# Optimization experiments

Measured on AMD Instinct MI355X. Metric: run time of the kernel, lower is better.

## Reference

```python
import jax, jax.numpy as jnp
import numpy as np

DIM = 32
NUM_BLOCKS = 6
XP_DIM = 16
TP_DIM = 8


def _init_lin(key, fan_in, fan_out):
    kw, kb = jax.random.split(key)
    s = 1.0 / np.sqrt(fan_in)
    W = jax.random.uniform(kw, (fan_in, fan_out), jnp.float32, -s, s)
    b = jax.random.uniform(kb, (fan_out,), jnp.float32, -s, s)
    return W, b


def setup_inputs() -> dict:
    key = jax.random.key(0)
    ks = jax.random.split(key, 24)
    B, N = 16, 256
    inp = {
        'coords': jax.random.normal(ks[0], (B, N, 2), jnp.float32),
        'x_params': jax.random.normal(ks[1], (B, 8, 2), jnp.float32),
        't_params': jax.random.normal(ks[2], (B, TP_DIM), jnp.float32),
    }
    # xp2ex: DNN([16,32,32],'sin')
    inp['xp2ex_W1'], inp['xp2ex_b1'] = _init_lin(ks[3], XP_DIM, DIM)
    inp['xp2ex_W2'], inp['xp2ex_b2'] = _init_lin(ks[4], DIM, DIM)
    # tp2et: DNN([8,32,32],'sin')
    inp['tp2et_W1'], inp['tp2et_b1'] = _init_lin(ks[5], TP_DIM, DIM)
    inp['tp2et_W2'], inp['tp2et_b2'] = _init_lin(ks[6], DIM, DIM)
    # initial hidden states (learnable; random instead of zeros for testing)
    inp['h0'] = 0.1 * jax.random.normal(ks[7], (1, DIM), jnp.float32)
    inp['gh0'] = 0.1 * jax.random.normal(ks[8], (1, DIM), jnp.float32)
    fWh, fbh, fWz, fbz = [], [], [], []
    for i in range(NUM_BLOCKS):
        W, b = _init_lin(ks[9 + i], DIM, DIM); fWh.append(W); fbh.append(b)
        W, b = _init_lin(jax.random.fold_in(ks[9 + i], 1), 2 + DIM, DIM); fWz.append(W); fbz.append(b)
    inp['f_Wh'], inp['f_bh'] = jnp.stack(fWh), jnp.stack(fbh)
    inp['f_Wz'], inp['f_bz'] = jnp.stack(fWz), jnp.stack(fbz)
    gWh, gbh, gWz, gbz = [], [], [], []
    for i in range(NUM_BLOCKS):
        W, b = _init_lin(ks[15 + i], DIM, DIM); gWh.append(W); gbh.append(b)
        W, b = _init_lin(jax.random.fold_in(ks[15 + i], 1), DIM + DIM, DIM); gWz.append(W); gbz.append(b)
    inp['g_Wh'], inp['g_bh'] = jnp.stack(gWh), jnp.stack(gbh)
    inp['g_Wz'], inp['g_bz'] = jnp.stack(gWz), jnp.stack(gbz)
    # d: SymmetricInitDNN([32,1],'identity') -> single linear
    inp['d_W'], inp['d_b'] = _init_lin(ks[21], DIM, 1)
    return inp


def reference(coords, x_params, t_params,
              xp2ex_W1, xp2ex_b1, xp2ex_W2, xp2ex_b2,
              tp2et_W1, tp2et_b1, tp2et_W2, tp2et_b2,
              h0, gh0,
              f_Wh, f_bh, f_Wz, f_bz,
              g_Wh, g_bh, g_Wz, g_bz,
              d_W, d_b):
    B, N = coords.shape[0], coords.shape[1]
    x = coords[..., 0:1]   # (B, N, 1)
    t = coords[..., 1:2]   # (B, N, 1)
    # conditioning embeddings (2-layer sin MLPs, linear output)
    xp = x_params.reshape(B, -1)                                   # (B, 16)
    ex = jnp.sin(xp @ xp2ex_W1 + xp2ex_b1) @ xp2ex_W2 + xp2ex_b2   # (B, 32)
    et = jnp.sin(t_params @ tp2et_W1 + tp2et_b1) @ tp2et_W2 + tp2et_b2  # (B, 32)
    # broadcast to (B, Nt, Nx, .) grid
    tr = jnp.broadcast_to(t[:, :, None, :], (B, N, N, 1))
    xr = jnp.broadcast_to(x[:, None, :, :], (B, N, N, 1))
    etu = jnp.broadcast_to(et[:, None, None, :], (B, N, N, DIM))
    ztpx = jnp.concatenate([xr, tr, etu], axis=-1)  # (B, N, N, 34)

    def block_step(h, w):
        Wh, bh, Wz, bz = w
        return jnp.sin(h @ Wh + bh + h_cond @ Wz + bz), None

    # f-stream: modulated-SIREN blocks conditioned on (x, t, et)
    h_cond = ztpx
    h = jnp.broadcast_to(h0[None, None], (B, N, N, DIM))
    h, _ = jax.lax.scan(block_step, h, (f_Wh, f_bh, f_Wz, f_bz))
    # g-stream: conditioned on (h, ex)
    ex_b = jnp.broadcast_to(ex[:, None, None, :], (B, N, N, DIM))
    h_cond = jnp.concatenate([h, ex_b], axis=-1)  # (B, N, N, 64)
    gh = jnp.broadcast_to(gh0[None, None], (B, N, N, DIM))
    gh, _ = jax.lax.scan(block_step, gh, (g_Wh, g_bh, g_Wz, g_bz))
    u_pred = gh @ d_W + d_b  # (B, N, N, 1)
    return u_pred
```

## Files before the change

kernel.cpp:

```cpp
#include <hip/hip_runtime.h>

#define DIM 32
#define NB  6
#define INV2PI 0.15915494309189535f

typedef __attribute__((ext_vector_type(8)))  _Float16 half8;
typedef __attribute__((ext_vector_type(16))) float floatx16;

union H8I4 { half8 h; int i[4]; };

__device__ __forceinline__ int pkrne(float a, float b) {
    _Float16 h0 = (_Float16)a, h1 = (_Float16)b;
    unsigned short u0, u1;
    __builtin_memcpy(&u0, &h0, 2); __builtin_memcpy(&u1, &h1, 2);
    return (int)(u0 | ((unsigned)u1 << 16));
}
#if __has_builtin(__builtin_amdgcn_cvt_pkrtz)
__device__ __forceinline__ int pkrtz(float a, float b) {
    auto h = __builtin_amdgcn_cvt_pkrtz(a, b);
    int r; __builtin_memcpy(&r, &h, 4); return r;
}
#else
#define pkrtz pkrne
#endif

__device__ __forceinline__ int Pmap(int s, int h, int j) { return 16*s + 8*(j>>2) + 4*h + (j&3); }
__device__ __forceinline__ int Qmap(int p)               { int r = p & 15, h = p >> 4; return 8*(r>>2) + 4*h + (r&3); }

#define MFMA(a, b, c) __builtin_amdgcn_mfma_f32_32x32x16_f16((a), (b), (c), 0, 0, 0)

__device__ __forceinline__ void sinsplit(const floatx16& acc, half8& b1, half8& b2) {
    H8I4 n1, n2;
    #pragma unroll
    for (int q = 0; q < 4; ++q) {
        n1.i[q] = pkrtz(__builtin_amdgcn_sinf(acc[2*q]),
                        __builtin_amdgcn_sinf(acc[2*q+1]));
        n2.i[q] = pkrtz(__builtin_amdgcn_sinf(acc[8+2*q]),
                        __builtin_amdgcn_sinf(acc[8+2*q+1]));
    }
    b1 = n1.h; b2 = n2.h;
}

#define LDS_BYTES 40064

__global__ __launch_bounds__(512, 4) void sep_mfma(
    const float* __restrict__ coords,
    const float* __restrict__ x_params,
    const float* __restrict__ t_params,
    const float* __restrict__ xW1, const float* __restrict__ xb1,
    const float* __restrict__ xW2, const float* __restrict__ xb2,
    const float* __restrict__ tW1, const float* __restrict__ tb1,
    const float* __restrict__ tW2, const float* __restrict__ tb2,
    const float* __restrict__ h0,  const float* __restrict__ gh0,
    const float* __restrict__ f_Wh, const float* __restrict__ f_bh,
    const float* __restrict__ f_Wz, const float* __restrict__ f_bz,
    const float* __restrict__ g_Wh, const float* __restrict__ g_bh,
    const float* __restrict__ g_Wz, const float* __restrict__ g_bz,
    const float* __restrict__ d_W,  const float* __restrict__ d_b,
    float* __restrict__ out)
{
    extern __shared__ char smem[];
    float* sdWp   = (float*)smem;
    float* shx    = sdWp + 32;
    float* sht    = shx + 32;
    float* sex    = sht + 32;
    float* set_   = sex + 32;
    unsigned short* sImg  = (unsigned short*)(set_ + 32);
    unsigned short* sInj  = sImg + 16384;
    unsigned short* sGnj  = sInj + 1536;
    unsigned short* sZero = sGnj + 1536;

    const int tid = threadIdx.x;
    const int b   = blockIdx.x >> 6;
    const int ig  = (blockIdx.x >> 1) & 31;
    const int jg  = blockIdx.x & 1;

    if (tid < 32) {
        float a = xb1[tid];
        for (int k = 0; k < 16; ++k) a = fmaf(x_params[b * 16 + k], xW1[k * 32 + tid], a);
        shx[tid] = __sinf(a);
    } else if (tid < 64) {
        int d = tid - 32;
        float a = tb1[d];
        for (int k = 0; k < 8; ++k) a = fmaf(t_params[b * 8 + k], tW1[k * 32 + d], a);
        sht[d] = __sinf(a);
    }
    if (tid < 128) ((int*)sZero)[tid] = 0;
    {
        int* sImgI = (int*)sImg;
        for (int ii = tid; ii < 8192; ii += 512) {
            int region = ii >> 9;
            int r = ii & 511;
            int s = r >> 8, t = r & 255;
            int lane = t >> 2, jj2 = t & 3;
            int m = lane & 31, hg = lane >> 5;
            int c0 = 16*s + 8*(jj2 >> 1) + 4*hg + 2*(jj2 & 1);
            float w0, w1;
            if (region < 5)       { int l = region + 1;  w0 = f_Wh[(l*32 + c0)*32 + m]; w1 = f_Wh[(l*32 + c0 + 1)*32 + m]; }
            else if (region < 10) { int l = region - 4;  w0 = g_Wh[(l*32 + c0)*32 + m]; w1 = g_Wh[(l*32 + c0 + 1)*32 + m]; }
            else                  { int l = region - 10; w0 = g_Wz[(l*64 + c0)*32 + m]; w1 = g_Wz[(l*64 + c0 + 1)*32 + m]; }
            sImgI[ii] = pkrne(w0 * INV2PI, w1 * INV2PI);
        }
    }
    __syncthreads();

    if (tid < 32) {
        float a0 = xb2[tid], a1 = 0.f, a2 = 0.f, a3 = 0.f;
        #pragma unroll
        for (int c = 0; c < 32; c += 4) {
            a0 = fmaf(shx[c],     xW2[(c)     * 32 + tid], a0);
            a1 = fmaf(shx[c + 1], xW2[(c + 1) * 32 + tid], a1);
            a2 = fmaf(shx[c + 2], xW2[(c + 2) * 32 + tid], a2);
            a3 = fmaf(shx[c + 3], xW2[(c + 3) * 32 + tid], a3);
        }
        sex[tid] = (a0 + a1) + (a2 + a3);
    } else if (tid < 64) {
        int d = tid - 32;
        float a0 = tb2[d], a1 = 0.f, a2 = 0.f, a3 = 0.f;
        #pragma unroll
        for (int c = 0; c < 32; c += 4) {
            a0 = fmaf(sht[c],     tW2[(c)     * 32 + d], a0);
            a1 = fmaf(sht[c + 1], tW2[(c + 1) * 32 + d], a1);
            a2 = fmaf(sht[c + 2], tW2[(c + 2) * 32 + d], a2);
            a3 = fmaf(sht[c + 3], tW2[(c + 3) * 32 + d], a3);
        }
        set_[d] = (a0 + a1) + (a2 + a3);
    }
    if (tid < 192) {
        int l = tid >> 5, m = tid & 31;
        float z0 = f_Wz[(l * 34 + 0) * 32 + m] * INV2PI;
        float z1 = f_Wz[(l * 34 + 1) * 32 + m] * INV2PI;
        _Float16 h0_ = (_Float16)z0; float z0h = (float)h0_, z0l = z0 - z0h;
        _Float16 h1_ = (_Float16)z1; float z1h = (float)h1_, z1l = z1 - z1h;
        int* p = (int*)sInj + 4 * tid;
        p[0] = pkrne(z0h, z0h);
        p[1] = pkrne(z0l, z1h);
        p[2] = pkrne(z1h, z1l);
        int* q = (int*)sGnj + 4 * tid;
        q[0] = 0; q[1] = 0; q[2] = 0;
    }
    if (tid < 32) sdWp[tid] = d_W[Qmap(tid)];
    __syncthreads();

    if (tid < 192) {
        int l = tid >> 5, m = tid & 31;
        float a0 = f_bh[l * 32 + m] + f_bz[l * 32 + m], a1 = 0.f, a2 = 0.f, a3 = 0.f;
        #pragma unroll
        for (int c = 0; c < 32; c += 4) {
            a0 = fmaf(set_[c],     f_Wz[(l * 34 + 2 + c) * 32 + m], a0);
            a1 = fmaf(set_[c + 1], f_Wz[(l * 34 + 3 + c) * 32 + m], a1);
            a2 = fmaf(set_[c + 2], f_Wz[(l * 34 + 4 + c) * 32 + m], a2);
            a3 = fmaf(set_[c + 3], f_Wz[(l * 34 + 5 + c) * 32 + m], a3);
        }
        float a = (a0 + a1) + (a2 + a3);
        if (l == 0) {
            float b0 = 0.f, b1 = 0.f, b2 = 0.f, b3 = 0.f;
            #pragma unroll
            for (int c = 0; c < 32; c += 4) {
                b0 = fmaf(h0[c],     f_Wh[(c)     * 32 + m], b0);
                b1 = fmaf(h0[c + 1], f_Wh[(c + 1) * 32 + m], b1);
                b2 = fmaf(h0[c + 2], f_Wh[(c + 2) * 32 + m], b2);
                b3 = fmaf(h0[c + 3], f_Wh[(c + 3) * 32 + m], b3);
            }
            a += (b0 + b1) + (b2 + b3);
        }
        a *= INV2PI;
        _Float16 aH_ = (_Float16)a; float aH = (float)aH_, aL = a - aH;
        ((int*)sInj)[4 * tid + 3] = pkrne(aH, aL);

        float g0 = g_bh[l * 32 + m] + g_bz[l * 32 + m], g1 = 0.f, g2 = 0.f, g3 = 0.f;
        #pragma unroll
        for (int c = 0; c < 32; c += 4) {
            g0 = fmaf(sex[c],     g_Wz[(l * 64 + 32 + c)     * 32 + m], g0);
            g1 = fmaf(sex[c + 1], g_Wz[(l * 64 + 32 + c + 1) * 32 + m], g1);
            g2 = fmaf(sex[c + 2], g_Wz[(l * 64 + 32 + c + 2) * 32 + m], g2);
            g3 = fmaf(sex[c + 3], g_Wz[(l * 64 + 32 + c + 3) * 32 + m], g3);
        }
        float g = (g0 + g1) + (g2 + g3);
        if (l == 0) {
            float c0_ = 0.f, c1_ = 0.f, c2_ = 0.f, c3_ = 0.f;
            #pragma unroll
            for (int c = 0; c < 32; c += 4) {
                c0_ = fmaf(gh0[c],     g_Wh[(c)     * 32 + m], c0_);
                c1_ = fmaf(gh0[c + 1], g_Wh[(c + 1) * 32 + m], c1_);
                c2_ = fmaf(gh0[c + 2], g_Wh[(c + 2) * 32 + m], c2_);
                c3_ = fmaf(gh0[c + 3], g_Wh[(c + 3) * 32 + m], c3_);
            }
            g += (c0_ + c1_) + (c2_ + c3_);
        }
        g *= INV2PI;
        _Float16 gH_ = (_Float16)g; float gH = (float)gH_, gL = g - gH;
        ((int*)sGnj)[4 * tid + 3] = pkrne(gH, gL);
    }
    __syncthreads();

    const int lane = tid & 63, wave = tid >> 6;
    const int i = ig * 8 + wave;
    const int e = lane & 31, hk = lane >> 5;
    const int pb = hk * 16;
    const float ti = coords[(b * 256 + i) * 2 + 1];
    const float db = d_b[0];

    float th_, tl_;
    { _Float16 h = (_Float16)ti; th_ = (float)h; tl_ = ti - th_; }

    const unsigned short* injbase = hk ? sZero : (sInj + e * 8);
    const unsigned short* gnjbase = hk ? sZero : (sGnj + e * 8);
    const int injstep = hk ? 0 : 256;

    floatx16 zc;
    #pragma unroll
    for (int r = 0; r < 16; ++r) zc[r] = 0.0f;

    #pragma unroll 1
    for (int t = 0; t < 4; ++t) {
        const int tile = jg * 4 + t;
        const int j = tile * 32 + e;
        const float xj = coords[(b * 256 + j) * 2];

        float xh_, xl_;
        { _Float16 h = (_Float16)xj; xh_ = (float)h; xl_ = xj - xh_; }
        H8I4 xtb;
        xtb.i[0] = pkrtz(xh_, xl_);
        xtb.i[1] = pkrtz(xh_, th_);
        xtb.i[2] = pkrtz(tl_, th_);
        xtb.i[3] = 0x3C003C00;
        const half8 xtB = xtb.h;

        floatx16 acc;
        half8 hB1, hB2;
        const unsigned short* ip = injbase;
        const unsigned short* gp = gnjbase;

        {
            half8 ia = *(const half8*)ip; ip += injstep;
            acc = MFMA(ia, xtB, zc);
            sinsplit(acc, hB1, hB2);
        }
        for (int l = 1; l < NB; ++l) {
            __builtin_amdgcn_sched_barrier(0);
            const unsigned short* base = &sImg[((l - 1) * 2) * 512 + lane * 8];
            half8 ia  = *(const half8*)ip; ip += injstep;
            half8 ah0 = *(const half8*)(base);
            half8 ah1 = *(const half8*)(base + 512);
            floatx16 z;
            z = MFMA(ia, xtB, zc);
            z = MFMA(ah0, hB1, z);
            acc = MFMA(ah1, hB2, z);
            sinsplit(acc, hB1, hB2);
        }

        half8 gB1, gB2;
        {
            __builtin_amdgcn_sched_barrier(0);
            const unsigned short* bz = &sImg[10240 + lane * 8];
            half8 gi  = *(const half8*)gp; gp += injstep;
            half8 wz0 = *(const half8*)(bz);
            half8 wz1 = *(const half8*)(bz + 512);
            floatx16 z;
            z = MFMA(gi, xtB, zc);
            z = MFMA(wz0, hB1, z);
            acc = MFMA(wz1, hB2, z);
            sinsplit(acc, gB1, gB2);
        }
        for (int l = 1; l < NB; ++l) {
            __builtin_amdgcn_sched_barrier(0);
            const unsigned short* bz = &sImg[10240 + (l * 2) * 512 + lane * 8];
            const unsigned short* bh = &sImg[5120 + ((l - 1) * 2) * 512 + lane * 8];
            half8 gi  = *(const half8*)gp; gp += injstep;
            half8 wz0 = *(const half8*)(bz);
            half8 wz1 = *(const half8*)(bz + 512);
            half8 wh0 = *(const half8*)(bh);
            half8 wh1 = *(const half8*)(bh + 512);
            floatx16 z;
            z = MFMA(gi, xtB, zc);
            z = MFMA(wz0, hB1, z);
            z = MFMA(wz1, hB2, z);
            z = MFMA(wh0, gB1, z);
            acc = MFMA(wh1, gB2, z);
            if (l < NB - 1) sinsplit(acc, gB1, gB2);
        }

        float u = 0.0f;
        #pragma unroll
        for (int r = 0; r < 16; ++r) u = fmaf(__builtin_amdgcn_sinf(acc[r]), sdWp[pb + r], u);
        u += __shfl_xor(u, 32);
        if (hk == 0) out[(b * 256 + i) * 256 + j] = u + db;
    }
}

extern "C" void kernel_launch(void* const* d_in, const int* in_sizes, int n_in,
                              void* d_out, int out_size, void* d_ws, size_t ws_size,
                              hipStream_t stream) {
    const float* coords   = (const float*)d_in[0];
    const float* x_params = (const float*)d_in[1];
    const float* t_params = (const float*)d_in[2];
    const float* xW1 = (const float*)d_in[3];
    const float* xb1 = (const float*)d_in[4];
    const float* xW2 = (const float*)d_in[5];
    const float* xb2 = (const float*)d_in[6];
    const float* tW1 = (const float*)d_in[7];
    const float* tb1 = (const float*)d_in[8];
    const float* tW2 = (const float*)d_in[9];
    const float* tb2 = (const float*)d_in[10];
    const float* h0  = (const float*)d_in[11];
    const float* gh0 = (const float*)d_in[12];
    const float* f_Wh = (const float*)d_in[13];
    const float* f_bh = (const float*)d_in[14];
    const float* f_Wz = (const float*)d_in[15];
    const float* f_bz = (const float*)d_in[16];
    const float* g_Wh = (const float*)d_in[17];
    const float* g_bh = (const float*)d_in[18];
    const float* g_Wz = (const float*)d_in[19];
    const float* g_bz = (const float*)d_in[20];
    const float* d_W  = (const float*)d_in[21];
    const float* d_b  = (const float*)d_in[22];

    hipFuncSetAttribute((const void*)sep_mfma,
                        hipFuncAttributeMaxDynamicSharedMemorySize, LDS_BYTES);

    sep_mfma<<<1024, 512, LDS_BYTES, stream>>>(
        coords, x_params, t_params, xW1, xb1, xW2, xb2, tW1, tb1, tW2, tb2,
        h0, gh0, f_Wh, f_bh, f_Wz, f_bz, g_Wh, g_bh, g_Wz, g_bz, d_W, d_b,
        (float*)d_out);
}
```

Measured before the change: 153.7 us.

## Interleave two independent column tiles per wave to hide MFMA and sin latency

Each block now covers all 256 columns of a row group, so the grid is halved and the per-block LDS weight setup is amortised over twice as much work. Inside the loop each wave processes two 32-column tiles, A and B, whose MFMA chains and sin activations are interleaved so the two dependency chains overlap. The injection MFMA is moved to the end of each chain. Launch bounds drop to 2 blocks per SM, which allows more registers for the doubled accumulators but lowers occupancy and gives fewer blocks for load balance.

After: 148.8 us. 3.2% less time.

```diff
diff --git a/kernel.cpp b/kernel.cpp
--- a/kernel.cpp
+++ b/kernel.cpp
@@ -43,7 +43,7 @@
 
 #define LDS_BYTES 40064
 
-__global__ __launch_bounds__(512, 4) void sep_mfma(
+__global__ __launch_bounds__(512, 2) void sep_mfma(
     const float* __restrict__ coords,
     const float* __restrict__ x_params,
     const float* __restrict__ t_params,
@@ -71,9 +71,8 @@
     unsigned short* sZero = sGnj + 1536;
 
     const int tid = threadIdx.x;
-    const int b   = blockIdx.x >> 6;
-    const int ig  = (blockIdx.x >> 1) & 31;
-    const int jg  = blockIdx.x & 1;
+    const int b   = blockIdx.x >> 5;
+    const int ig  = blockIdx.x & 31;
 
     if (tid < 32) {
         float a = xb1[tid];
@@ -208,84 +207,114 @@
     const unsigned short* gnjbase = hk ? sZero : (sGnj + e * 8);
     const int injstep = hk ? 0 : 256;
 
-    floatx16 zc;
-    #pragma unroll
-    for (int r = 0; r < 16; ++r) zc[r] = 0.0f;
-
     #pragma unroll 1
     for (int t = 0; t < 4; ++t) {
-        const int tile = jg * 4 + t;
-        const int j = tile * 32 + e;
-        const float xj = coords[(b * 256 + j) * 2];
-
-        float xh_, xl_;
-        { _Float16 h = (_Float16)xj; xh_ = (float)h; xl_ = xj - xh_; }
-        H8I4 xtb;
-        xtb.i[0] = pkrtz(xh_, xl_);
-        xtb.i[1] = pkrtz(xh_, th_);
-        xtb.i[2] = pkrtz(tl_, th_);
-        xtb.i[3] = 0x3C003C00;
-        const half8 xtB = xtb.h;
-
-        floatx16 acc;
-        half8 hB1, hB2;
+        const int jA = (2 * t) * 32 + e;
+        const int jB = jA + 32;
+        const float xjA = coords[(b * 256 + jA) * 2];
+        const float xjB = coords[(b * 256 + jB) * 2];
+
+        half8 btA, btB;
+        {
+            float xh_, xl_;
+            { _Float16 h = (_Float16)xjA; xh_ = (float)h; xl_ = xjA - xh_; }
+            H8I4 u;
+            u.i[0] = pkrtz(xh_, xl_);
+            u.i[1] = pkrtz(xh_, th_);
+            u.i[2] = pkrtz(tl_, th_);
+            u.i[3] = 0x3C003C00;
+            btA = u.h;
+            { _Float16 h = (_Float16)xjB; xh_ = (float)h; xl_ = xjB - xh_; }
+            u.i[0] = pkrtz(xh_, xl_);
+            u.i[1] = pkrtz(xh_, th_);
+            u.i[2] = pkrtz(tl_, th_);
+            u.i[3] = 0x3C003C00;
+            btB = u.h;
+        }
+
+        floatx16 accA, accB;
+        half8 hA1, hA2, hB1, hB2;
         const unsigned short* ip = injbase;
         const unsigned short* gp = gnjbase;
 
         {
             half8 ia = *(const half8*)ip; ip += injstep;
-            acc = MFMA(ia, xtB, zc);
-            sinsplit(acc, hB1, hB2);
+            floatx16 zA, zB;
+            #pragma unroll
+            for (int r = 0; r < 16; ++r) { zA[r] = 0.0f; zB[r] = 0.0f; }
+            accA = MFMA(ia, btA, zA);
+            accB = MFMA(ia, btB, zB);
+            sinsplit(accA, hA1, hA2);
+            sinsplit(accB, hB1, hB2);
         }
         for (int l = 1; l < NB; ++l) {
             __builtin_amdgcn_sched_barrier(0);
             const unsigned short* base = &sImg[((l - 1) * 2) * 512 + lane * 8];
-            half8 ia  = *(const half8*)ip; ip += injstep;
             half8 ah0 = *(const half8*)(base);
             half8 ah1 = *(const half8*)(base + 512);
-            floatx16 z;
-            z = MFMA(ia, xtB, zc);
-            z = MFMA(ah0, hB1, z);
-            acc = MFMA(ah1, hB2, z);
-            sinsplit(acc, hB1, hB2);
-        }
-
-        half8 gB1, gB2;
+            half8 ia  = *(const half8*)ip; ip += injstep;
+            floatx16 zA, zB;
+            #pragma unroll
+            for (int r = 0; r < 16; ++r) { zA[r] = 0.0f; zB[r] = 0.0f; }
+            zA = MFMA(ah0, hA1, zA);  zB = MFMA(ah0, hB1, zB);
+            zA = MFMA(ah1, hA2, zA);  zB = MFMA(ah1, hB2, zB);
+            accA = MFMA(ia, btA, zA); accB = MFMA(ia, btB, zB);
+            sinsplit(accA, hA1, hA2);
+            sinsplit(accB, hB1, hB2);
+        }
+
+        half8 gA1, gA2, gB1, gB2;
         {
             __builtin_amdgcn_sched_barrier(0);
             const unsigned short* bz = &sImg[10240 + lane * 8];
-            half8 gi  = *(const half8*)gp; gp += injstep;
             half8 wz0 = *(const half8*)(bz);
             half8 wz1 = *(const half8*)(bz + 512);
-            floatx16 z;
-            z = MFMA(gi, xtB, zc);
-            z = MFMA(wz0, hB1, z);
-            acc = MFMA(wz1, hB2, z);
-            sinsplit(acc, gB1, gB2);
+            half8 gi  = *(const half8*)gp; gp += injstep;
+            floatx16 zA, zB;
+            #pragma unroll
+            for (int r = 0; r < 16; ++r) { zA[r] = 0.0f; zB[r] = 0.0f; }
+            zA = MFMA(wz0, hA1, zA);  zB = MFMA(wz0, hB1, zB);
+            zA = MFMA(wz1, hA2, zA);  zB = MFMA(wz1, hB2, zB);
+            accA = MFMA(gi, btA, zA); accB = MFMA(gi, btB, zB);
+            sinsplit(accA, gA1, gA2);
+            sinsplit(accB, gB1, gB2);
         }
         for (int l = 1; l < NB; ++l) {
             __builtin_amdgcn_sched_barrier(0);
             const unsigned short* bz = &sImg[10240 + (l * 2) * 512 + lane * 8];
             const unsigned short* bh = &sImg[5120 + ((l - 1) * 2) * 512 + lane * 8];
-            half8 gi  = *(const half8*)gp; gp += injstep;
             half8 wz0 = *(const half8*)(bz);
             half8 wz1 = *(const half8*)(bz + 512);
             half8 wh0 = *(const half8*)(bh);
             half8 wh1 = *(const half8*)(bh + 512);
-            floatx16 z;
-            z = MFMA(gi, xtB, zc);
-            z = MFMA(wz0, hB1, z);
-            z = MFMA(wz1, hB2, z);
-            z = MFMA(wh0, gB1, z);
-            acc = MFMA(wh1, gB2, z);
-            if (l < NB - 1) sinsplit(acc, gB1, gB2);
-        }
-
-        float u = 0.0f;
-        #pragma unroll
-        for (int r = 0; r < 16; ++r) u = fmaf(__builtin_amdgcn_sinf(acc[r]), sdWp[pb + r], u);
-        u += __shfl_xor(u, 32);
-        if (hk == 0) out[(b * 256 + i) * 256 + j] = u + db;
+            half8 gi  = *(const half8*)gp; gp += injstep;
+            floatx16 zA, zB;
+            #pragma unroll
+            for (int r = 0; r < 16; ++r) { zA[r] = 0.0f; zB[r] = 0.0f; }
+            zA = MFMA(wz0, hA1, zA);  zB = MFMA(wz0, hB1, zB);
+            zA = MFMA(wz1, hA2, zA);  zB = MFMA(wz1, hB2, zB);
+            zA = MFMA(wh0, gA1, zA);  zB = MFMA(wh0, gB1, zB);
+            zA = MFMA(wh1, gA2, zA);  zB = MFMA(wh1, gB2, zB);
+            accA = MFMA(gi, btA, zA); accB = MFMA(gi, btB, zB);
+            if (l < NB - 1) {
+                sinsplit(accA, gA1, gA2);
+                sinsplit(accB, gB1, gB2);
+            }
+        }
+
+        float uA = 0.0f, uB = 0.0f;
+        #pragma unroll
+        for (int r = 0; r < 16; ++r) {
+            float w = sdWp[pb + r];
+            uA = fmaf(__builtin_amdgcn_sinf(accA[r]), w, uA);
+            uB = fmaf(__builtin_amdgcn_sinf(accB[r]), w, uB);
+        }
+        uA += __shfl_xor(uA, 32);
+        uB += __shfl_xor(uB, 32);
+        if (hk == 0) {
+            out[(b * 256 + i) * 256 + jA] = uA + db;
+            out[(b * 256 + i) * 256 + jB] = uB + db;
+        }
     }
 }
 
@@ -319,7 +348,7 @@
     hipFuncSetAttribute((const void*)sep_mfma,
                         hipFuncAttributeMaxDynamicSharedMemorySize, LDS_BYTES);
 
-    sep_mfma<<<1024, 512, LDS_BYTES, stream>>>(
+    sep_mfma<<<512, 512, LDS_BYTES, stream>>>(
         coords, x_params, t_params, xW1, xb1, xW2, xb2, tW1, tb1, tW2, tb2,
         h0, gh0, f_Wh, f_bh, f_Wz, f_bz, g_Wh, g_bh, g_Wz, g_bz, d_W, d_b,
         (float*)d_out);
```
